# Optimization experiments

Measured on AMD Instinct MI355X. Metric: run time of the kernel, lower is better.

## Reference

```python
import jax, jax.numpy as jnp
import numpy as np

# Fixed graph/model dims (see shape_source)
C = 16      # cardinality
SUB = 64    # representation_size // cardinality
R = 1024    # representation_size
E = 1024    # node_encoding_size
S = 1024    # processed spatial feature size
G = 256     # global (FPN) channels
NH = 64     # number of human nodes
N = 256     # total number of nodes (humans first)
P = NH * N  # number of (human, node) pairs
EPS = 1e-5


def _layernorm(x, g, b):
    mu = jnp.mean(x, axis=-1, keepdims=True)
    var = jnp.var(x, axis=-1, keepdims=True)
    return (x - mu) * jax.lax.rsqrt(var + EPS) * g + b


def _pair_head(app, spat, W1, b1, W2, b2, W3, b3):
    # app: [P_or_1, A], spat: [P, S] -> [P, R]  (sum over cardinality; NO outer relu)
    a1 = jnp.einsum('pi,cis->cps', app, W1) + b1[:, None, :]   # [C,P_or_1,SUB]
    a2 = jnp.einsum('pj,cjs->cps', spat, W2) + b2[:, None, :]  # [C,P,SUB]
    h = jax.nn.relu(a1 * a2)                                   # broadcast over P
    return jnp.einsum('cps,csr->pr', h, W3) + jnp.sum(b3, axis=0)


def reference(node_encodings, spatial_raw, global_feat,
              sp_W1, sp_b1, sp_W2, sp_b2, sp_W3, sp_b3,
              ah_W1, ah_b1, ah_W2, ah_b2, ah_W3, ah_b3,
              o2s_W1, o2s_b1, o2s_W2, o2s_b2, o2s_W3, o2s_b3,
              s2o_W1, s2o_b1, s2o_W2, s2o_b2, s2o_W3, s2o_b3,
              ahg_W1, ahg_b1, ahg_W2, ahg_b2, ahg_W3, ahg_b3,
              adj_W, adj_b, lnh_g, lnh_b, lno_g, lno_b):
    # spatial head MLP: 36 -> 128 -> 256 -> 1024 with ReLU
    sp = jax.nn.relu(spatial_raw @ sp_W1 + sp_b1)
    sp = jax.nn.relu(sp @ sp_W2 + sp_b2)
    sp = jax.nn.relu(sp @ sp_W3 + sp_b3)            # [P, S]
    sp3 = sp.reshape(NH, N, S)                      # [NH, N, S]

    x_idx = jnp.repeat(jnp.arange(NH), N)           # [P]
    y_idx = jnp.tile(jnp.arange(N), NH)             # [P]

    h_enc = node_encodings[:NH]                     # humans are permuted to the top
    o_enc = node_encodings

    for _ in range(1):  # num_iter
        app_pairs = jnp.concatenate([h_enc[x_idx], o_enc[y_idx]], axis=1)  # [P, 2E]
        weights = jax.nn.relu(_pair_head(app_pairs, sp, ah_W1, ah_b1, ah_W2, ah_b2, ah_W3, ah_b3))
        adj = (weights @ adj_W + adj_b).reshape(NH, N)

        # obj_to_sub (node_type='object'): appearance = all node encodings
        a1 = jnp.einsum('ni,cis->cns', o_enc, o2s_W1) + o2s_b1[:, None, :]          # [C,N,SUB]
        a2 = jnp.einsum('hnj,cjs->chns', sp3, o2s_W2) + o2s_b2[:, None, None, :]    # [C,NH,N,SUB]
        m = jnp.einsum('chns,csr->hnr', jax.nn.relu(a1[:, None] * a2), o2s_W3) + jnp.sum(o2s_b3, axis=0)
        msg_h = jax.nn.relu(jnp.sum(jax.nn.softmax(adj, axis=1)[..., None] * m, axis=1))  # [NH,R]
        h_enc = _layernorm(h_enc + msg_h, lnh_g, lnh_b)

        # sub_to_obj (node_type='human'): appearance = human encodings
        a1 = jnp.einsum('hi,cis->chs', h_enc, s2o_W1) + s2o_b1[:, None, :]          # [C,NH,SUB]
        a2 = jnp.einsum('hnj,cjs->cnhs', sp3, s2o_W2) + s2o_b2[:, None, None, :]    # [C,N,NH,SUB]
        m = jnp.einsum('cnhs,csr->nhr', jax.nn.relu(a1[:, None] * a2), s2o_W3) + jnp.sum(s2o_b3, axis=0)
        msg_o = jax.nn.relu(jnp.sum(jax.nn.softmax(adj.T, axis=1)[..., None] * m, axis=1))  # [N,R]
        o_enc = _layernorm(o_enc + msg_o, lno_g, lno_b)

    app_final = jnp.concatenate([h_enc[x_idx], o_enc[y_idx]], axis=1)               # [P, 2E]
    f_local = jax.nn.relu(_pair_head(app_final, sp, ah_W1, ah_b1, ah_W2, ah_b2, ah_W3, ah_b3))
    f_glob = jax.nn.relu(_pair_head(global_feat, sp, ahg_W1, ahg_b1, ahg_W2, ahg_b2, ahg_W3, ahg_b3))
    return jnp.concatenate([f_local, f_glob], axis=1)  # [P, 2R]


def setup_inputs() -> dict:
    key = jax.random.key(0)
    ks = iter(jax.random.split(key, 64))
    def rn(shape, scale=0.05):
        return jax.random.normal(next(ks), shape, dtype=jnp.float32) * scale
    inp = {
        'node_encodings': jax.random.normal(next(ks), (N, E), dtype=jnp.float32),
        'spatial_raw': jax.random.normal(next(ks), (P, 36), dtype=jnp.float32),
        'global_feat': jax.random.normal(next(ks), (1, G), dtype=jnp.float32),
        'sp_W1': rn((36, 128)), 'sp_b1': jnp.zeros(128, jnp.float32),
        'sp_W2': rn((128, 256)), 'sp_b2': jnp.zeros(256, jnp.float32),
        'sp_W3': rn((256, S)), 'sp_b3': jnp.zeros(S, jnp.float32),
        'ah_W1': rn((C, 2 * E, SUB)), 'ah_b1': jnp.zeros((C, SUB), jnp.float32),
        'ah_W2': rn((C, S, SUB)), 'ah_b2': jnp.zeros((C, SUB), jnp.float32),
        'ah_W3': rn((C, SUB, R)), 'ah_b3': jnp.zeros((C, R), jnp.float32),
        'o2s_W1': rn((C, E, SUB)), 'o2s_b1': jnp.zeros((C, SUB), jnp.float32),
        'o2s_W2': rn((C, S, SUB)), 'o2s_b2': jnp.zeros((C, SUB), jnp.float32),
        'o2s_W3': rn((C, SUB, R)), 'o2s_b3': jnp.zeros((C, R), jnp.float32),
        's2o_W1': rn((C, E, SUB)), 's2o_b1': jnp.zeros((C, SUB), jnp.float32),
        's2o_W2': rn((C, S, SUB)), 's2o_b2': jnp.zeros((C, SUB), jnp.float32),
        's2o_W3': rn((C, SUB, R)), 's2o_b3': jnp.zeros((C, R), jnp.float32),
        'ahg_W1': rn((C, G, SUB)), 'ahg_b1': jnp.zeros((C, SUB), jnp.float32),
        'ahg_W2': rn((C, S, SUB)), 'ahg_b2': jnp.zeros((C, SUB), jnp.float32),
        'ahg_W3': rn((C, SUB, R)), 'ahg_b3': jnp.zeros((C, R), jnp.float32),
        'adj_W': rn((R, 1)), 'adj_b': jnp.zeros(1, jnp.float32),
        'lnh_g': jnp.ones(E, jnp.float32), 'lnh_b': jnp.zeros(E, jnp.float32),
        'lno_g': jnp.ones(E, jnp.float32), 'lno_b': jnp.zeros(E, jnp.float32),
    }
    return inp
```

## Files before the change

kernel.cpp:

```cpp
#include <hip/hip_runtime.h>
#include <hip/hip_bf16.h>
#include <stdint.h>
#include <stddef.h>

using bf16 = __hip_bfloat16;
typedef __bf16 bf16x8 __attribute__((ext_vector_type(8)));
typedef float f32x4 __attribute__((ext_vector_type(4)));

#define P_  16384

__device__ __forceinline__ void gload16(const void* g, void* l) {
    __builtin_amdgcn_global_load_lds((const __attribute__((address_space(1))) void*)g,
                                     (__attribute__((address_space(3))) void*)l, 16, 0, 0);
}

struct GArgs {
    const bf16* A; const bf16* B; void* C;
    const float* bias;
    const float* aux1;
    int M, N, K, ldc, kchunk;
    void* dst1; void* dst2; void* dst3; void* dstH;
    const float* cb0; const float* cb1; const float* cb2; const float* cb3;
    const float* a1gv; const float* Ahp; const float* Aop; const float* b1p;
};

template<int MODE, bool RELU, bool BIAS>
__global__ __launch_bounds__(256, 4)
void gemm_bt(GArgs g)
{
    __shared__ __align__(16) bf16 As[128 * 64];
    __shared__ __align__(16) bf16 Bs[128 * 64];

    const int tid  = threadIdx.x;
    const int wave = tid >> 6;
    const int lane = tid & 63;
    const int tileM = blockIdx.x * 128;
    const int tileN = blockIdx.y * 128;
    const int wr = (wave >> 1) << 6;
    const int wc = (wave & 1) << 6;
    const int M = g.M, N = g.N, K = g.K;

    const bf16* Ap = g.A; const bf16* Bp = g.B;
    void* Cp = g.C; const float* biasp = g.bias;
    if (MODE == 0 && blockIdx.z == 1) {
        Ap = (const bf16*)g.dst1; Bp = (const bf16*)g.dst2;
        Cp = g.dst3; biasp = g.cb1;
    }

    f32x4 acc[4][4] = {};

    const int gk = (((lane & 7) ^ (lane >> 3)) << 3);
    int arow[4], brow[4];
    #pragma unroll
    for (int j = 0; j < 4; ++j) {
        int r = wave * 32 + j * 8 + (lane >> 3);
        int gr = tileM + r; if (gr > M - 1) gr = M - 1; arow[j] = gr;
        int gn = tileN + r; if (gn > N - 1) gn = N - 1; brow[j] = gn;
    }
    const int m0 = wr + (lane & 15);
    const int n0 = wc + (lane & 15);
    const int q  = lane >> 4;

    int kbeg = 0, kend = K;
    if constexpr (MODE == 2) { kbeg = blockIdx.z * 64; kend = kbeg + 64; }

    for (int k0 = kbeg; k0 < kend; k0 += 64) {
        #pragma unroll
        for (int j = 0; j < 4; ++j) {
            int c = wave * 256 + j * 64 + lane;
            gload16(Ap + (size_t)arow[j] * K + k0 + gk, (void*)(As + c * 8));
            gload16(Bp + (size_t)brow[j] * K + k0 + gk, (void*)(Bs + c * 8));
        }
        __syncthreads();
        #pragma unroll
        for (int kk = 0; kk < 2; ++kk) {
            const int gs = ((kk << 2) + q) ^ (lane & 7);
            bf16x8 af[4], bfv[4];
            #pragma unroll
            for (int i = 0; i < 4; ++i) {
                af[i]  = *(const bf16x8*)(As + (m0 + i * 16) * 64 + gs * 8);
                bfv[i] = *(const bf16x8*)(Bs + (n0 + i * 16) * 64 + gs * 8);
            }
            #pragma unroll
            for (int i = 0; i < 4; ++i)
                #pragma unroll
                for (int j = 0; j < 4; ++j)
                    acc[i][j] = __builtin_amdgcn_mfma_f32_16x16x32_bf16(af[i], bfv[j], acc[i][j], 0, 0, 0);
        }
        __syncthreads();
    }

    const int rbase = tileM + wr + ((lane >> 4) << 2);
    const int cbase = tileN + wc + (lane & 15);

    if constexpr (MODE == 0 || MODE == 1) {
        #pragma unroll
        for (int i = 0; i < 4; ++i)
            #pragma unroll
            for (int j = 0; j < 4; ++j)
                #pragma unroll
                for (int r = 0; r < 4; ++r) {
                    int grow = rbase + i * 16 + r;
                    if (grow >= M) continue;
                    int gcol = cbase + j * 16;
                    float v = acc[i][j][r];
                    if (BIAS) v += biasp[gcol];
                    if (RELU) v = fmaxf(v, 0.f);
                    if (MODE == 1) ((bf16*)Cp)[(size_t)grow * g.ldc + gcol] = __float2bfloat16(v);
                    else           ((float*)Cp)[(size_t)grow * g.ldc + gcol] = v;
                }
    } else if constexpr (MODE == 2) {
        #pragma unroll
        for (int i = 0; i < 4; ++i)
            #pragma unroll
            for (int j = 0; j < 4; ++j)
                #pragma unroll
                for (int r = 0; r < 4; ++r) {
                    int grow = rbase + i * 16 + r;
                    if (grow >= M) continue;
                    atomicAdd((float*)Cp + (size_t)grow * g.ldc + cbase + j * 16, acc[i][j][r]);
                }
    } else if constexpr (MODE == 6) {
        #pragma unroll
        for (int i = 0; i < 4; ++i)
            #pragma unroll
            for (int r = 0; r < 4; ++r) {
                float s = 0.f;
                #pragma unroll
                for (int j = 0; j < 4; ++j) {
                    int gcol = cbase + j * 16;
                    s += fmaxf(acc[i][j][r] + biasp[gcol], 0.f) * g.aux1[gcol];
                }
                s += __shfl_xor(s, 1); s += __shfl_xor(s, 2);
                s += __shfl_xor(s, 4); s += __shfl_xor(s, 8);
                if ((lane & 15) == 0)
                    atomicAdd((float*)Cp + rbase + i * 16 + r, s);
            }
    } else if constexpr (MODE == 9) {
        int grp = tileN >> 10;
        int lcb = (tileN & 1023) + wc + (lane & 15);
        #pragma unroll
        for (int i = 0; i < 4; ++i)
            #pragma unroll
            for (int j = 0; j < 4; ++j)
                #pragma unroll
                for (int r = 0; r < 4; ++r) {
                    int p    = rbase + i * 16 + r;
                    int lcol = lcb + j * 16;
                    float accv = acc[i][j][r];
                    if (grp == 0) {
                        bf16 a2b = __float2bfloat16(accv + g.cb0[lcol]);
                        ((bf16*)Cp)[(size_t)p * 1024 + lcol] = a2b;
                        float a1 = g.Ahp[((size_t)(p >> 8)) * 3072 + lcol]
                                 + g.Aop[((size_t)(p & 255)) * 3072 + lcol] + g.b1p[lcol];
                        ((bf16*)g.dstH)[(size_t)p * 1024 + lcol] =
                            __float2bfloat16(fmaxf(a1 * (float)a2b, 0.f));
                    } else if (grp == 1) {
                        ((bf16*)g.dst1)[(size_t)p * 1024 + lcol] =
                            __float2bfloat16(accv + g.cb1[lcol]);
                    } else if (grp == 2) {
                        ((bf16*)g.dst2)[(size_t)p * 1024 + lcol] =
                            __float2bfloat16(accv + g.cb2[lcol]);
                    } else {
                        float a2v = accv + g.cb3[lcol];
                        ((bf16*)g.dst3)[(size_t)p * 1024 + lcol] =
                            __float2bfloat16(fmaxf(g.a1gv[lcol] * a2v, 0.f));
                    }
                }
    }
}

static GArgs mkargs(const bf16* A, const bf16* B, void* C, const float* bias,
                    const float* aux1, int M, int N, int K, int ldc, int kchunk)
{
    GArgs g{};
    g.A = A; g.B = B; g.C = C; g.bias = bias; g.aux1 = aux1;
    g.M = M; g.N = N; g.K = K; g.ldc = ldc; g.kchunk = kchunk;
    return g;
}

__global__ void reduce_o2s(const bf16* __restrict__ a2, const float* __restrict__ a1,
                           const float* __restrict__ b1, const float* __restrict__ sh,
                           bf16* __restrict__ out)
{
    int h = blockIdx.y, cq = blockIdx.x;
    int ng = threadIdx.x >> 5, ct = threadIdx.x & 31;
    int c = cq * 256 + ct * 8;
    float b1v[8], accv[8] = {};
    #pragma unroll
    for (int j = 0; j < 8; ++j) b1v[j] = b1[c + j];
    const float* shh = sh + h * 256;
    for (int n = ng; n < 256; n += 8) {
        float w = shh[n];
        bf16x8 a2v = *(const bf16x8*)(a2 + ((size_t)(h * 256 + n) << 10) + c);
        const float* a1p = a1 + (size_t)n * 3072 + c;
        #pragma unroll
        for (int j = 0; j < 8; ++j)
            accv[j] += w * fmaxf((a1p[j] + b1v[j]) * (float)a2v[j], 0.f);
    }
    __shared__ float red[8][264];
    #pragma unroll
    for (int j = 0; j < 8; ++j) red[ng][ct * 8 + j] = accv[j];
    __syncthreads();
    for (int s = 4; s > 0; s >>= 1) {
        if (ng < s)
            #pragma unroll
            for (int j = 0; j < 8; ++j) red[ng][ct * 8 + j] += red[ng + s][ct * 8 + j];
        __syncthreads();
    }
    if (ng == 0) {
        bf16x8 o;
        #pragma unroll
        for (int j = 0; j < 8; ++j) o[j] = (__bf16)red[0][ct * 8 + j];
        *(bf16x8*)(out + (size_t)h * 1024 + c) = o;
    }
}

__global__ void reduce_s2o(const bf16* __restrict__ a2, const float* __restrict__ a1,
                           const float* __restrict__ b1, const float* __restrict__ so,
                           bf16* __restrict__ out)
{
    int n = blockIdx.y, cq = blockIdx.x;
    int hg = threadIdx.x >> 5, ct = threadIdx.x & 31;
    int c = cq * 256 + ct * 8;
    float b1v[8], accv[8] = {};
    #pragma unroll
    for (int j = 0; j < 8; ++j) b1v[j] = b1[c + j];
    const float* son = so + n * 64;
    #pragma unroll
    for (int hh = 0; hh < 8; ++hh) {
        int h = hg + hh * 8;
        float w = son[h];
        bf16x8 a2v = *(const bf16x8*)(a2 + ((size_t)(h * 256 + n) << 10) + c);
        const float* a1p = a1 + (size_t)h * 2048 + c;
        #pragma unroll
        for (int j = 0; j < 8; ++j)
            accv[j] += w * fmaxf((a1p[j] + b1v[j]) * (float)a2v[j], 0.f);
    }
    __shared__ float red[8][264];
    #pragma unroll
    for (int j = 0; j < 8; ++j) red[hg][ct * 8 + j] = accv[j];
    __syncthreads();
    for (int s = 4; s > 0; s >>= 1) {
        if (hg < s)
            #pragma unroll
            for (int j = 0; j < 8; ++j) red[hg][ct * 8 + j] += red[hg + s][ct * 8 + j];
        __syncthreads();
    }
    if (hg == 0) {
        bf16x8 o;
        #pragma unroll
        for (int j = 0; j < 8; ++j) o[j] = (__bf16)red[0][ct * 8 + j];
        *(bf16x8*)(out + (size_t)n * 1024 + c) = o;
    }
}

__global__ void transp(const float* __restrict__ src, bf16* __restrict__ dst,
                       int rows, int cols, size_t sstride, size_t dstride)
{
    const float* s = src + blockIdx.z * sstride;
    bf16*        d = dst + blockIdx.z * dstride;
    __shared__ float tile[32][33];
    int c0 = blockIdx.x * 32, r0 = blockIdx.y * 32;
    int x = threadIdx.x, y = threadIdx.y;
    for (int yy = y; yy < 32; yy += 8) {
        int r = r0 + yy, c = c0 + x;
        tile[yy][x] = (r < rows && c < cols) ? s[(size_t)r * cols + c] : 0.f;
    }
    __syncthreads();
    for (int yy = y; yy < 32; yy += 8) {
        int c = c0 + yy, r = r0 + x;
        if (c < cols && r < rows) d[(size_t)c * rows + r] = __float2bfloat16(tile[x][yy]);
    }
}

struct T9 { const float* s[9]; bf16* d[9]; size_t ss[9]; };
__global__ void transp64b(T9 t)
{
    int pair = blockIdx.z >> 4, slice = blockIdx.z & 15;
    const float* s = t.s[pair] + slice * t.ss[pair];
    bf16*        d = t.d[pair] + slice * 65536;
    __shared__ float tile[32][33];
    int c0 = blockIdx.x * 32, r0 = blockIdx.y * 32;
    int x = threadIdx.x, y = threadIdx.y;
    for (int yy = y; yy < 32; yy += 8)
        tile[yy][x] = s[(size_t)(r0 + yy) * 64 + c0 + x];
    __syncthreads();
    for (int yy = y; yy < 32; yy += 8)
        d[(size_t)(c0 + yy) * 1024 + r0 + x] = __float2bfloat16(tile[x][yy]);
}

struct T4 { const float* s[4]; bf16* d[4]; };
__global__ void transp1024b(T4 t)
{
    const float* s = t.s[blockIdx.z];
    bf16*        d = t.d[blockIdx.z];
    __shared__ float tile[32][33];
    int c0 = blockIdx.x * 32, r0 = blockIdx.y * 32;
    int x = threadIdx.x, y = threadIdx.y;
    for (int yy = y; yy < 32; yy += 8)
        tile[yy][x] = s[(size_t)(r0 + yy) * 1024 + c0 + x];
    __syncthreads();
    for (int yy = y; yy < 32; yy += 8)
        d[(size_t)(c0 + yy) * 1024 + r0 + x] = __float2bfloat16(tile[x][yy]);
}

__global__ void conv_spw1(const float* __restrict__ src, bf16* __restrict__ dst) {
    int i = blockIdx.x * 256 + threadIdx.x;
    if (i >= 128 * 64) return;
    int k = i & 63, n = i >> 6;
    dst[i] = __float2bfloat16(k < 36 ? src[k * 128 + n] : 0.f);
}

__global__ void pad_spatial(const float* __restrict__ src, bf16* __restrict__ dst) {
    int i = blockIdx.x * 256 + threadIdx.x;
    int k = i & 63, p = i >> 6;
    dst[i] = __float2bfloat16(k < 36 ? src[p * 36 + k] : 0.f);
}

__global__ void cast_f2b(const float* __restrict__ src, bf16* __restrict__ dst, int n) {
    int i = blockIdx.x * 256 + threadIdx.x;
    if (i < n) dst[i] = __float2bfloat16(src[i]);
}

struct S4 { const float* s[4]; float* d[4]; };
__global__ void sumb3b(S4 a) {
    int i = blockIdx.x * 256 + threadIdx.x;
    int pair = i >> 10, r = i & 1023;
    const float* b3 = a.s[pair];
    float s = 0.f;
    #pragma unroll
    for (int c = 0; c < 16; ++c) s += b3[c * 1024 + r];
    a.d[pair][r] = s;
}

__global__ void hbuild(const float* __restrict__ Ah, int ah_ld,
                       const float* __restrict__ Ao, int ao_ld,
                       const float* __restrict__ b1, const bf16* __restrict__ a2,
                       bf16* __restrict__ H)
{
    size_t base = ((size_t)blockIdx.x * 256 + threadIdx.x) * 8;
    int cs = (int)(base & 1023);
    int p  = (int)(base >> 10);
    const float* ph = Ah + (size_t)(p >> 8) * ah_ld + cs;
    const float* po = Ao + (size_t)(p & 255) * ao_ld + cs;
    bf16x8 av = *(const bf16x8*)(a2 + base);
    bf16x8 o;
    #pragma unroll
    for (int j = 0; j < 8; ++j) {
        float a1 = ph[j] + po[j] + b1[cs + j];
        o[j] = (__bf16)fmaxf(a1 * (float)av[j], 0.f);
    }
    *(bf16x8*)(H + base) = o;
}

__global__ void softmax_h(const float* __restrict__ adj, float* __restrict__ sh) {
    int h = blockIdx.x, n = threadIdx.x;
    __shared__ float red[256];
    float v = adj[h * 256 + n];
    red[n] = v; __syncthreads();
    for (int s = 128; s > 0; s >>= 1) { if (n < s) red[n] = fmaxf(red[n], red[n + s]); __syncthreads(); }
    float m = red[0]; __syncthreads();
    float e = expf(v - m);
    red[n] = e; __syncthreads();
    for (int s = 128; s > 0; s >>= 1) { if (n < s) red[n] += red[n + s]; __syncthreads(); }
    sh[h * 256 + n] = e / red[0];
}

__global__ void softmax_o(const float* __restrict__ adj, float* __restrict__ so) {
    int n = blockIdx.x, h = threadIdx.x;
    float v = adj[h * 256 + n];
    float m = v;
    #pragma unroll
    for (int off = 32; off; off >>= 1) m = fmaxf(m, __shfl_xor(m, off));
    float e = expf(v - m);
    float s = e;
    #pragma unroll
    for (int off = 32; off; off >>= 1) s += __shfl_xor(s, off);
    so[n * 64 + h] = e / s;
}

__global__ void ln_k(const float* __restrict__ x, const float* __restrict__ msgraw,
                     const float* __restrict__ sb3,
                     const float* __restrict__ g, const float* __restrict__ bb,
                     bf16* __restrict__ out)
{
    int row = blockIdx.x, t = threadIdx.x;
    const float* xr = x + (size_t)row * 1024;
    const float* mr = msgraw + (size_t)row * 1024;
    float v[4]; float s = 0.f, ss = 0.f;
    #pragma unroll
    for (int j = 0; j < 4; ++j) {
        int i = t + j * 256;
        v[j] = xr[i] + fmaxf(mr[i] + sb3[i], 0.f);
        s += v[j]; ss += v[j] * v[j];
    }
    __shared__ float r1[256], r2[256];
    r1[t] = s; r2[t] = ss; __syncthreads();
    for (int k = 128; k > 0; k >>= 1) { if (t < k) { r1[t] += r1[t + k]; r2[t] += r2[t + k]; } __syncthreads(); }
    float mean = r1[0] * (1.f / 1024.f);
    float var  = r2[0] * (1.f / 1024.f) - mean * mean;
    float inv  = rsqrtf(var + 1e-5f);
    #pragma unroll
    for (int j = 0; j < 4; ++j) {
        int i = t + j * 256;
        out[(size_t)row * 1024 + i] = __float2bfloat16((v[j] - mean) * inv * g[i] + bb[i]);
    }
}

__global__ void a1g_k(const float* __restrict__ gf, const float* __restrict__ W1,
                      const float* __restrict__ b1, float* __restrict__ a1g)
{
    int cs = blockIdx.x * 256 + threadIdx.x;
    int c = cs >> 6, s = cs & 63;
    float acc = b1[cs];
    for (int g = 0; g < 256; ++g) acc += gf[g] * W1[((size_t)c * 256 + g) * 64 + s];
    a1g[cs] = acc;
}

extern "C" void kernel_launch(void* const* d_in, const int* in_sizes, int n_in,
                              void* d_out, int out_size, void* d_ws, size_t ws_size,
                              hipStream_t stream)
{
    const float* node_enc = (const float*)d_in[0];
    const float* spatial  = (const float*)d_in[1];
    const float* gfeat    = (const float*)d_in[2];
    const float* sp_W1 = (const float*)d_in[3];  const float* sp_b1 = (const float*)d_in[4];
    const float* sp_W2 = (const float*)d_in[5];  const float* sp_b2 = (const float*)d_in[6];
    const float* sp_W3 = (const float*)d_in[7];  const float* sp_b3 = (const float*)d_in[8];
    const float* ah_W1 = (const float*)d_in[9];  const float* ah_b1 = (const float*)d_in[10];
    const float* ah_W2 = (const float*)d_in[11]; const float* ah_b2 = (const float*)d_in[12];
    const float* ah_W3 = (const float*)d_in[13]; const float* ah_b3 = (const float*)d_in[14];
    const float* o2s_W1 = (const float*)d_in[15]; const float* o2s_b1 = (const float*)d_in[16];
    const float* o2s_W2 = (const float*)d_in[17]; const float* o2s_b2 = (const float*)d_in[18];
    const float* o2s_W3 = (const float*)d_in[19]; const float* o2s_b3 = (const float*)d_in[20];
    const float* s2o_W1 = (const float*)d_in[21]; const float* s2o_b1 = (const float*)d_in[22];
    const float* s2o_W2 = (const float*)d_in[23]; const float* s2o_b2 = (const float*)d_in[24];
    const float* s2o_W3 = (const float*)d_in[25]; const float* s2o_b3 = (const float*)d_in[26];
    const float* ahg_W1 = (const float*)d_in[27]; const float* ahg_b1 = (const float*)d_in[28];
    const float* ahg_W2 = (const float*)d_in[29]; const float* ahg_b2 = (const float*)d_in[30];
    const float* ahg_W3 = (const float*)d_in[31]; const float* ahg_b3 = (const float*)d_in[32];
    const float* adj_W = (const float*)d_in[33];
    const float* lnh_g = (const float*)d_in[35]; const float* lnh_b = (const float*)d_in[36];
    const float* lno_g = (const float*)d_in[37]; const float* lno_b = (const float*)d_in[38];

    char* w = (char*)d_ws;
    auto alloc = [&](size_t bytes) { char* p = w; w += (bytes + 255) & ~(size_t)255; return p; };
    bf16*  sp      = (bf16*)alloc((size_t)P_ * 1024 * 2);
    bf16*  a2_ah   = (bf16*)alloc((size_t)P_ * 1024 * 2);
    bf16*  Hbuf    = (bf16*)alloc((size_t)P_ * 1024 * 2);
    bf16*  a2_o2s  = (bf16*)alloc((size_t)P_ * 1024 * 2);
    bf16*  a2_s2o  = (bf16*)alloc((size_t)P_ * 1024 * 2);
    bf16*  H_ahg   = (bf16*)alloc((size_t)P_ * 1024 * 2);
    bf16*  spat_pad= (bf16*)alloc((size_t)P_ * 64 * 2);
    bf16*  spL1    = (bf16*)alloc((size_t)P_ * 128 * 2);
    bf16*  spL2    = (bf16*)alloc((size_t)P_ * 256 * 2);
    bf16*  enc_bf  = (bf16*)alloc(256 * 1024 * 2);
    bf16*  henc_bf = (bf16*)alloc(64 * 1024 * 2);
    bf16*  oenc_bf = (bf16*)alloc(256 * 1024 * 2);
    bf16*  HredH   = (bf16*)alloc(64 * 1024 * 2);
    bf16*  HredO   = (bf16*)alloc(256 * 1024 * 2);
    bf16*  spW1t   = (bf16*)alloc(128 * 64 * 2);
    bf16*  spW2t   = (bf16*)alloc(256 * 128 * 2);
    bf16*  spW3t   = (bf16*)alloc(1024 * 256 * 2);
    bf16*  W2cat   = (bf16*)alloc((size_t)4096 * 1024 * 2);
    bf16*  W1cat3  = (bf16*)alloc((size_t)3072 * 1024 * 2);
    bf16*  W1catF  = (bf16*)alloc((size_t)2048 * 1024 * 2);
    bf16*  ahW3t   = (bf16*)alloc(1024 * 1024 * 2);
    bf16*  o2sW3t  = (bf16*)alloc(1024 * 1024 * 2);
    bf16*  s2oW3t  = (bf16*)alloc(1024 * 1024 * 2);
    bf16*  ahgW3t  = (bf16*)alloc(1024 * 1024 * 2);
    float* Aoa1x = (float*)alloc(256 * 3072 * 4);
    float* A1f   = (float*)alloc(64 * 2048 * 4);
    float* Ao_f  = (float*)alloc(256 * 1024 * 4);
    size_t z1_bytes = (size_t)(256 * 3072 + 64 * 2048 + 256 * 1024) * 4 + 1024;
    float* adjv  = (float*)alloc(P_ * 4);
    float* msgh  = (float*)alloc(64 * 1024 * 4);
    float* msgo  = (float*)alloc(256 * 1024 * 4);
    size_t z2_bytes = (size_t)(P_ + 64 * 1024 + 256 * 1024) * 4 + 1024;
    float* sh    = (float*)alloc(P_ * 4);
    float* so    = (float*)alloc(P_ * 4);
    float* a1g   = (float*)alloc(1024 * 4);
    float* sb3_ah  = (float*)alloc(4096);
    float* sb3_o2s = (float*)alloc(4096);
    float* sb3_s2o = (float*)alloc(4096);
    float* sb3_ahg = (float*)alloc(4096);

    hipMemsetAsync(Aoa1x, 0, z1_bytes, stream);
    hipMemsetAsync(adjv,  0, z2_bytes, stream);

    {
        T9 t;
        t.s[0] = ah_W1;                     t.d[0] = W1cat3 + (size_t)2048 * 1024; t.ss[0] = (size_t)2048 * 64;
        t.s[1] = ah_W1 + (size_t)1024 * 64; t.d[1] = W1cat3;                       t.ss[1] = (size_t)2048 * 64;
        t.s[2] = o2s_W1;                    t.d[2] = W1cat3 + (size_t)1024 * 1024; t.ss[2] = 65536;
        t.s[3] = s2o_W1;                    t.d[3] = W1catF;                       t.ss[3] = 65536;
        t.s[4] = ah_W1;                     t.d[4] = W1catF + (size_t)1024 * 1024; t.ss[4] = (size_t)2048 * 64;
        t.s[5] = ah_W2;                     t.d[5] = W2cat;                        t.ss[5] = 65536;
        t.s[6] = o2s_W2;                    t.d[6] = W2cat + (size_t)1024 * 1024;  t.ss[6] = 65536;
        t.s[7] = s2o_W2;                    t.d[7] = W2cat + (size_t)2048 * 1024;  t.ss[7] = 65536;
        t.s[8] = ahg_W2;                    t.d[8] = W2cat + (size_t)3072 * 1024;  t.ss[8] = 65536;
        transp64b<<<dim3(2, 32, 144), dim3(32, 8), 0, stream>>>(t);
    }
    {
        T4 t;
        t.s[0] = ah_W3;  t.d[0] = ahW3t;
        t.s[1] = o2s_W3; t.d[1] = o2sW3t;
        t.s[2] = s2o_W3; t.d[2] = s2oW3t;
        t.s[3] = ahg_W3; t.d[3] = ahgW3t;
        transp1024b<<<dim3(32, 32, 4), dim3(32, 8), 0, stream>>>(t);
    }
    dim3 tb(32, 8);
    conv_spw1<<<32, 256, 0, stream>>>(sp_W1, spW1t);
    transp<<<dim3(8, 4, 1),  tb, 0, stream>>>(sp_W2, spW2t, 128, 256, 0, 0);
    transp<<<dim3(32, 8, 1), tb, 0, stream>>>(sp_W3, spW3t, 256, 1024, 0, 0);
    pad_spatial<<<4096, 256, 0, stream>>>(spatial, spat_pad);
    cast_f2b<<<1024, 256, 0, stream>>>(node_enc, enc_bf, 256 * 1024);
    {
        S4 a;
        a.s[0] = ah_b3;  a.d[0] = sb3_ah;
        a.s[1] = o2s_b3; a.d[1] = sb3_o2s;
        a.s[2] = s2o_b3; a.d[2] = sb3_s2o;
        a.s[3] = ahg_b3; a.d[3] = sb3_ahg;
        sumb3b<<<16, 256, 0, stream>>>(a);
    }
    a1g_k<<<4, 256, 0, stream>>>(gfeat, ahg_W1, ahg_b1, a1g);

    gemm_bt<2, false, false><<<dim3(2, 24, 16), 256, 0, stream>>>(
        mkargs(enc_bf, W1cat3, Aoa1x, nullptr, nullptr, 256, 3072, 1024, 3072, 64));

    gemm_bt<1, true, true><<<dim3(128, 1), 256, 0, stream>>>(
        mkargs(spat_pad, spW1t, spL1, sp_b1, nullptr, P_, 128, 64, 128, 0));
    gemm_bt<1, true, true><<<dim3(128, 2), 256, 0, stream>>>(
        mkargs(spL1, spW2t, spL2, sp_b2, nullptr, P_, 256, 128, 256, 0));
    gemm_bt<1, true, true><<<dim3(128, 8), 256, 0, stream>>>(
        mkargs(spL2, spW3t, sp, sp_b3, nullptr, P_, 1024, 256, 1024, 0));

    {
        GArgs g = mkargs(sp, W2cat, a2_ah, nullptr, nullptr, P_, 4096, 1024, 1024, 0);
        g.dst1 = a2_o2s; g.dst2 = a2_s2o; g.dst3 = H_ahg; g.dstH = Hbuf;
        g.cb0 = ah_b2; g.cb1 = o2s_b2; g.cb2 = s2o_b2; g.cb3 = ahg_b2;
        g.a1gv = a1g; g.Ahp = Aoa1x + 2048; g.Aop = Aoa1x; g.b1p = ah_b1;
        gemm_bt<9, false, false><<<dim3(128, 32), 256, 0, stream>>>(g);
    }

    gemm_bt<6, false, false><<<dim3(128, 8), 256, 0, stream>>>(
        mkargs(Hbuf, ahW3t, adjv, sb3_ah, adj_W, P_, 1024, 1024, 1024, 0));
    softmax_h<<<64, 256, 0, stream>>>(adjv, sh);
    softmax_o<<<256, 64, 0, stream>>>(adjv, so);

    reduce_o2s<<<dim3(4, 64), 256, 0, stream>>>(a2_o2s, Aoa1x + 1024, o2s_b1, sh, HredH);
    gemm_bt<2, false, false><<<dim3(1, 8, 16), 256, 0, stream>>>(
        mkargs(HredH, o2sW3t, msgh, nullptr, nullptr, 64, 1024, 1024, 1024, 64));
    ln_k<<<64, 256, 0, stream>>>(node_enc, msgh, sb3_o2s, lnh_g, lnh_b, henc_bf);

    gemm_bt<2, false, false><<<dim3(1, 16, 16), 256, 0, stream>>>(
        mkargs(henc_bf, W1catF, A1f, nullptr, nullptr, 64, 2048, 1024, 2048, 64));

    reduce_s2o<<<dim3(4, 256), 256, 0, stream>>>(a2_s2o, A1f, s2o_b1, so, HredO);
    gemm_bt<2, false, false><<<dim3(2, 8, 16), 256, 0, stream>>>(
        mkargs(HredO, s2oW3t, msgo, nullptr, nullptr, 256, 1024, 1024, 1024, 64));
    ln_k<<<256, 256, 0, stream>>>(node_enc, msgo, sb3_s2o, lno_g, lno_b, oenc_bf);

    gemm_bt<2, false, false><<<dim3(2, 8, 16), 256, 0, stream>>>(
        mkargs(oenc_bf, W1cat3, Ao_f, nullptr, nullptr, 256, 1024, 1024, 1024, 64));
    hbuild<<<8192, 256, 0, stream>>>(A1f + 1024, 2048, Ao_f, 1024, ah_b1, a2_ah, Hbuf);

    {
        GArgs g = mkargs(Hbuf, ahW3t, (float*)d_out, sb3_ah, nullptr, P_, 1024, 1024, 2048, 0);
        g.dst1 = (void*)H_ahg; g.dst2 = (void*)ahgW3t;
        g.dst3 = (void*)((float*)d_out + 1024); g.cb1 = sb3_ahg;
        gemm_bt<0, true, true><<<dim3(128, 8, 2), 256, 0, stream>>>(g);
    }

    (void)in_sizes; (void)n_in; (void)out_size; (void)ws_size;
}
```

Before: 798.2 us.

## Fuse small prep and softmax launches, remap GEMM tile order, raise occupancy hint

Combines the spatial padding, encoding cast, sp_W1 conversion, b3 summation and a1g computation into one prep kernel, and merges the two softmax kernels into one launch. Two memsets become a single contiguous memset. The GEMM launch bound goes from 4 to 5 waves per SIMD, and the block index is remapped so consecutive workgroups spread across the grid, likely for XCD/L2 locality. The main risks are register spilling under the tighter launch bound and idle threads in the softmax_o branch, which now runs 256-thread blocks with only 64 active threads.

```diff
diff --git a/kernel.cpp b/kernel.cpp
--- a/kernel.cpp
+++ b/kernel.cpp
@@ -25,7 +25,7 @@
 };
 
 template<int MODE, bool RELU, bool BIAS>
-__global__ __launch_bounds__(256, 4)
+__global__ __launch_bounds__(256, 5)
 void gemm_bt(GArgs g)
 {
     __shared__ __align__(16) bf16 As[128 * 64];
@@ -34,8 +34,14 @@
     const int tid  = threadIdx.x;
     const int wave = tid >> 6;
     const int lane = tid & 63;
-    const int tileM = blockIdx.x * 128;
-    const int tileN = blockIdx.y * 128;
+
+    const int nx  = gridDim.x;
+    const int nwg = nx * gridDim.y;
+    int lin = blockIdx.y * nx + blockIdx.x;
+    if ((nwg & 7) == 0) lin = (lin & 7) * (nwg >> 3) + (lin >> 3);
+    const int tileM = (lin % nx) * 128;
+    const int tileN = (lin / nx) * 128;
+
     const int wr = (wave >> 1) << 6;
     const int wc = (wave & 1) << 6;
     const int M = g.M, N = g.N, K = g.K;
@@ -305,33 +311,44 @@
         d[(size_t)(c0 + yy) * 1024 + r0 + x] = __float2bfloat16(tile[x][yy]);
 }
 
-__global__ void conv_spw1(const float* __restrict__ src, bf16* __restrict__ dst) {
-    int i = blockIdx.x * 256 + threadIdx.x;
-    if (i >= 128 * 64) return;
-    int k = i & 63, n = i >> 6;
-    dst[i] = __float2bfloat16(k < 36 ? src[k * 128 + n] : 0.f);
-}
-
-__global__ void pad_spatial(const float* __restrict__ src, bf16* __restrict__ dst) {
-    int i = blockIdx.x * 256 + threadIdx.x;
-    int k = i & 63, p = i >> 6;
-    dst[i] = __float2bfloat16(k < 36 ? src[p * 36 + k] : 0.f);
-}
-
-__global__ void cast_f2b(const float* __restrict__ src, bf16* __restrict__ dst, int n) {
-    int i = blockIdx.x * 256 + threadIdx.x;
-    if (i < n) dst[i] = __float2bfloat16(src[i]);
-}
-
-struct S4 { const float* s[4]; float* d[4]; };
-__global__ void sumb3b(S4 a) {
-    int i = blockIdx.x * 256 + threadIdx.x;
-    int pair = i >> 10, r = i & 1023;
-    const float* b3 = a.s[pair];
-    float s = 0.f;
-    #pragma unroll
-    for (int c = 0; c < 16; ++c) s += b3[c * 1024 + r];
-    a.d[pair][r] = s;
+struct PrepArgs {
+    const float* spatial; bf16* spat_pad;
+    const float* node_enc; bf16* enc_bf;
+    const float* sp_W1; bf16* spW1t;
+    const float* b3s0; const float* b3s1; const float* b3s2; const float* b3s3;
+    float* b3d0; float* b3d1; float* b3d2; float* b3d3;
+    const float* gf; const float* ahgW1; const float* ahgb1; float* a1g;
+};
+__global__ void prep_k(PrepArgs a)
+{
+    int bid = blockIdx.x, tid = threadIdx.x;
+    if (bid < 4096) {
+        int i = bid * 256 + tid;
+        int k = i & 63, p = i >> 6;
+        a.spat_pad[i] = __float2bfloat16(k < 36 ? a.spatial[p * 36 + k] : 0.f);
+    } else if (bid < 5120) {
+        int i = (bid - 4096) * 256 + tid;
+        a.enc_bf[i] = __float2bfloat16(a.node_enc[i]);
+    } else if (bid < 5152) {
+        int i = (bid - 5120) * 256 + tid;
+        int k = i & 63, n = i >> 6;
+        a.spW1t[i] = __float2bfloat16(k < 36 ? a.sp_W1[k * 128 + n] : 0.f);
+    } else if (bid < 5168) {
+        int i = (bid - 5152) * 256 + tid;
+        int pair = i >> 10, r = i & 1023;
+        const float* b3 = (pair == 0) ? a.b3s0 : (pair == 1) ? a.b3s1 : (pair == 2) ? a.b3s2 : a.b3s3;
+        float*       bd = (pair == 0) ? a.b3d0 : (pair == 1) ? a.b3d1 : (pair == 2) ? a.b3d2 : a.b3d3;
+        float s = 0.f;
+        #pragma unroll
+        for (int c = 0; c < 16; ++c) s += b3[c * 1024 + r];
+        bd[r] = s;
+    } else {
+        int cs = (bid - 5168) * 256 + tid;
+        int c = cs >> 6, s = cs & 63;
+        float acc = a.ahgb1[cs];
+        for (int gg = 0; gg < 256; ++gg) acc += a.gf[gg] * a.ahgW1[((size_t)c * 256 + gg) * 64 + s];
+        a.a1g[cs] = acc;
+    }
 }
 
 __global__ void hbuild(const float* __restrict__ Ah, int ah_ld,
@@ -354,30 +371,35 @@
     *(bf16x8*)(H + base) = o;
 }
 
-__global__ void softmax_h(const float* __restrict__ adj, float* __restrict__ sh) {
-    int h = blockIdx.x, n = threadIdx.x;
-    __shared__ float red[256];
-    float v = adj[h * 256 + n];
-    red[n] = v; __syncthreads();
-    for (int s = 128; s > 0; s >>= 1) { if (n < s) red[n] = fmaxf(red[n], red[n + s]); __syncthreads(); }
-    float m = red[0]; __syncthreads();
-    float e = expf(v - m);
-    red[n] = e; __syncthreads();
-    for (int s = 128; s > 0; s >>= 1) { if (n < s) red[n] += red[n + s]; __syncthreads(); }
-    sh[h * 256 + n] = e / red[0];
-}
-
-__global__ void softmax_o(const float* __restrict__ adj, float* __restrict__ so) {
-    int n = blockIdx.x, h = threadIdx.x;
-    float v = adj[h * 256 + n];
-    float m = v;
-    #pragma unroll
-    for (int off = 32; off; off >>= 1) m = fmaxf(m, __shfl_xor(m, off));
-    float e = expf(v - m);
-    float s = e;
-    #pragma unroll
-    for (int off = 32; off; off >>= 1) s += __shfl_xor(s, off);
-    so[n * 64 + h] = e / s;
+__global__ void softmax_ho(const float* __restrict__ adj,
+                           float* __restrict__ sh, float* __restrict__ so)
+{
+    int bid = blockIdx.x;
+    if (bid < 64) {
+        int h = bid, n = threadIdx.x;
+        __shared__ float red[256];
+        float v = adj[h * 256 + n];
+        red[n] = v; __syncthreads();
+        for (int s = 128; s > 0; s >>= 1) { if (n < s) red[n] = fmaxf(red[n], red[n + s]); __syncthreads(); }
+        float m = red[0]; __syncthreads();
+        float e = expf(v - m);
+        red[n] = e; __syncthreads();
+        for (int s = 128; s > 0; s >>= 1) { if (n < s) red[n] += red[n + s]; __syncthreads(); }
+        sh[h * 256 + n] = e / red[0];
+    } else {
+        int n = bid - 64, h = threadIdx.x;
+        if (h < 64) {
+            float v = adj[h * 256 + n];
+            float m = v;
+            #pragma unroll
+            for (int off = 32; off; off >>= 1) m = fmaxf(m, __shfl_xor(m, off));
+            float e = expf(v - m);
+            float s = e;
+            #pragma unroll
+            for (int off = 32; off; off >>= 1) s += __shfl_xor(s, off);
+            so[n * 64 + h] = e / s;
+        }
+    }
 }
 
 __global__ void ln_k(const float* __restrict__ x, const float* __restrict__ msgraw,
@@ -406,16 +428,6 @@
         int i = t + j * 256;
         out[(size_t)row * 1024 + i] = __float2bfloat16((v[j] - mean) * inv * g[i] + bb[i]);
     }
-}
-
-__global__ void a1g_k(const float* __restrict__ gf, const float* __restrict__ W1,
-                      const float* __restrict__ b1, float* __restrict__ a1g)
-{
-    int cs = blockIdx.x * 256 + threadIdx.x;
-    int c = cs >> 6, s = cs & 63;
-    float acc = b1[cs];
-    for (int g = 0; g < 256; ++g) acc += gf[g] * W1[((size_t)c * 256 + g) * 64 + s];
-    a1g[cs] = acc;
 }
 
 extern "C" void kernel_launch(void* const* d_in, const int* in_sizes, int n_in,
@@ -473,11 +485,9 @@
     float* Aoa1x = (float*)alloc(256 * 3072 * 4);
     float* A1f   = (float*)alloc(64 * 2048 * 4);
     float* Ao_f  = (float*)alloc(256 * 1024 * 4);
-    size_t z1_bytes = (size_t)(256 * 3072 + 64 * 2048 + 256 * 1024) * 4 + 1024;
     float* adjv  = (float*)alloc(P_ * 4);
     float* msgh  = (float*)alloc(64 * 1024 * 4);
     float* msgo  = (float*)alloc(256 * 1024 * 4);
-    size_t z2_bytes = (size_t)(P_ + 64 * 1024 + 256 * 1024) * 4 + 1024;
     float* sh    = (float*)alloc(P_ * 4);
     float* so    = (float*)alloc(P_ * 4);
     float* a1g   = (float*)alloc(1024 * 4);
@@ -486,8 +496,7 @@
     float* sb3_s2o = (float*)alloc(4096);
     float* sb3_ahg = (float*)alloc(4096);
 
-    hipMemsetAsync(Aoa1x, 0, z1_bytes, stream);
-    hipMemsetAsync(adjv,  0, z2_bytes, stream);
+    hipMemsetAsync(Aoa1x, 0, (size_t)((char*)sh - (char*)Aoa1x), stream);
 
     {
         T9 t;
@@ -511,20 +520,18 @@
         transp1024b<<<dim3(32, 32, 4), dim3(32, 8), 0, stream>>>(t);
     }
     dim3 tb(32, 8);
-    conv_spw1<<<32, 256, 0, stream>>>(sp_W1, spW1t);
     transp<<<dim3(8, 4, 1),  tb, 0, stream>>>(sp_W2, spW2t, 128, 256, 0, 0);
     transp<<<dim3(32, 8, 1), tb, 0, stream>>>(sp_W3, spW3t, 256, 1024, 0, 0);
-    pad_spatial<<<4096, 256, 0, stream>>>(spatial, spat_pad);
-    cast_f2b<<<1024, 256, 0, stream>>>(node_enc, enc_bf, 256 * 1024);
     {
-        S4 a;
-        a.s[0] = ah_b3;  a.d[0] = sb3_ah;
-        a.s[1] = o2s_b3; a.d[1] = sb3_o2s;
-        a.s[2] = s2o_b3; a.d[2] = sb3_s2o;
-        a.s[3] = ahg_b3; a.d[3] = sb3_ahg;
-        sumb3b<<<16, 256, 0, stream>>>(a);
-    }
-    a1g_k<<<4, 256, 0, stream>>>(gfeat, ahg_W1, ahg_b1, a1g);
+        PrepArgs a;
+        a.spatial = spatial; a.spat_pad = spat_pad;
+        a.node_enc = node_enc; a.enc_bf = enc_bf;
+        a.sp_W1 = sp_W1; a.spW1t = spW1t;
+        a.b3s0 = ah_b3; a.b3s1 = o2s_b3; a.b3s2 = s2o_b3; a.b3s3 = ahg_b3;
+        a.b3d0 = sb3_ah; a.b3d1 = sb3_o2s; a.b3d2 = sb3_s2o; a.b3d3 = sb3_ahg;
+        a.gf = gfeat; a.ahgW1 = ahg_W1; a.ahgb1 = ahg_b1; a.a1g = a1g;
+        prep_k<<<5172, 256, 0, stream>>>(a);
+    }
 
     gemm_bt<2, false, false><<<dim3(2, 24, 16), 256, 0, stream>>>(
         mkargs(enc_bf, W1cat3, Aoa1x, nullptr, nullptr, 256, 3072, 1024, 3072, 64));
@@ -546,8 +553,7 @@
 
     gemm_bt<6, false, false><<<dim3(128, 8), 256, 0, stream>>>(
         mkargs(Hbuf, ahW3t, adjv, sb3_ah, adj_W, P_, 1024, 1024, 1024, 0));
-    softmax_h<<<64, 256, 0, stream>>>(adjv, sh);
-    softmax_o<<<256, 64, 0, stream>>>(adjv, so);
+    softmax_ho<<<320, 256, 0, stream>>>(adjv, sh, so);
 
     reduce_o2s<<<dim3(4, 64), 256, 0, stream>>>(a2_o2s, Aoa1x + 1024, o2s_b1, sh, HredH);
     gemm_bt<2, false, false><<<dim3(1, 8, 16), 256, 0, stream>>>(
```

After: 1.536 ms. 1.92x slower.
